# Optimization experiments

Measured on AMD Instinct MI355X. Metric: run time of the kernel, lower is better.

## Reference

```python
import jax, jax.numpy as jnp
import numpy as np

B, N, D, H, C = 32, 2048, 64, 4, 16  # batch, nodes, hidden, heads, per-head node-emb dim


def setup_inputs() -> dict:
    key = jax.random.key(0)
    ks = jax.random.split(key, 8)
    def w(k, shape):
        return jax.random.normal(k, shape, jnp.float32) * 0.05
    return {
        "hidden_state": jax.random.normal(ks[0], (B, N, D), jnp.float32),
        # predefined (row-normalized-ish) adjacencies; /N keeps 2-hop propagation magnitudes sane
        "A1": jax.random.uniform(ks[1], (N, N), jnp.float32) / N,
        "A2": jax.random.uniform(ks[2], (N, N), jnp.float32) / N,
        "E1": jax.random.normal(ks[3], (N, H, C), jnp.float32),
        "E2": jax.random.normal(ks[4], (N, H, C), jnp.float32),
        # GCNLayer mlp: Linear((gdep+1)*D, D) for z, r, c gates
        "Wz": w(ks[5], (3 * D, D)), "bz": jnp.zeros((D,), jnp.float32),
        "Wr": w(ks[6], (3 * D, D)), "br": jnp.zeros((D,), jnp.float32),
        "Wc": w(ks[7], (3 * D, D)), "bc": jnp.zeros((D,), jnp.float32),
        "w_pre": jnp.float32(0.5),
        "w_adp": jnp.float32(0.5),
    }


def _gcn2(A, x, W, b):
    h1 = jnp.einsum('wv,bvc->bwc', A, x)
    h2 = jnp.einsum('wv,bvc->bwc', A, h1)
    return jnp.concatenate([x, h1, h2], axis=-1) @ W + b


def _gcn3(A, x, W, b):
    # GCNLayer with per-head adjacency A:[H,N,N]; x broadcast to [B,H,N,D]
    h0 = jnp.broadcast_to(x[:, None], (x.shape[0], A.shape[0], x.shape[1], x.shape[2]))
    h1 = jnp.einsum('hwv,bhvc->bhwc', A, h0)
    h2 = jnp.einsum('hwv,bhvc->bhwc', A, h1)
    return jnp.concatenate([h0, h1, h2], axis=-1) @ W + b  # [B,H,N,D]


def reference(hidden_state, A1, A2, E1, E2, Wz, bz, Wr, br, Wc, bc, w_pre, w_adp):
    # adaptive attention-like adjacency: relu(E1 E2^T)/sqrt(c), softmax over v
    sqrt_c = jnp.sqrt(jnp.asarray(E1.shape[-1], jnp.float32))
    scores = jax.nn.relu(jnp.einsum('whc,vhc->hwv', E1, E2)) / sqrt_c  # [H,N,N]
    A_adp = jax.nn.softmax(scores, axis=-1)

    def gate(x, W, b):
        pre = _gcn2(A1, x, W, b) + _gcn2(A2, x, W, b)          # sum over predefined adjs
        adp = _gcn3(A_adp, x, W, b).mean(axis=1)               # mean over heads
        return w_pre * pre + w_adp * adp

    z = jax.nn.sigmoid(gate(hidden_state, Wz, bz))
    r = jax.nn.sigmoid(gate(hidden_state, Wr, br))
    c = jnp.tanh(gate(r * hidden_state, Wc, bc))
    return (1.0 - z) * hidden_state + z * c
```

## Files before the change

### kernel.cpp

```cpp
#include <hip/hip_runtime.h>

#define NNODE 2048
#define NBATCH 32

typedef __attribute__((ext_vector_type(4))) float f32x4;
typedef __attribute__((ext_vector_type(8))) __bf16 bf16x8;
typedef __attribute__((ext_vector_type(4))) __bf16 bf16x4;

__device__ __forceinline__ void gload16(const void* g, void* lds) {
  __builtin_amdgcn_global_load_lds(
      (const __attribute__((address_space(1))) unsigned int*)g,
      (__attribute__((address_space(3))) unsigned int*)lds, 16, 0, 0);
}

__global__ __launch_bounds__(256) void prep_ew(const float* __restrict__ E1,
                                               const float* __restrict__ E2,
                                               const float* __restrict__ Wz,
                                               const float* __restrict__ Wr,
                                               const float* __restrict__ Wc,
                                               const float* __restrict__ wpre,
                                               const float* __restrict__ wadp,
                                               __bf16* __restrict__ E1p,
                                               __bf16* __restrict__ E2p,
                                               __bf16* __restrict__ Wzrt,
                                               __bf16* __restrict__ Wct) {
  if (blockIdx.x < 128) {
    int idx = blockIdx.x * 256 + threadIdx.x;
    int cq = idx & 3;
    int n = (idx >> 2) & 2047;
    int h = idx >> 13;
    const float4 q1 = *(const float4*)(E1 + (size_t)(n * 4 + h) * 16 + cq * 4);
    const float4 q2 = *(const float4*)(E2 + (size_t)(n * 4 + h) * 16 + cq * 4);
    size_t o = ((size_t)h * NNODE + n) * 32 + cq * 4;
    E1p[o + 0] = (__bf16)q1.x; E1p[o + 1] = (__bf16)q1.y;
    E1p[o + 2] = (__bf16)q1.z; E1p[o + 3] = (__bf16)q1.w;
    E2p[o + 0] = (__bf16)q2.x; E2p[o + 1] = (__bf16)q2.y;
    E2p[o + 2] = (__bf16)q2.z; E2p[o + 3] = (__bf16)q2.w;
    size_t oz = o + 16;
    E1p[oz + 0] = (__bf16)0.f; E1p[oz + 1] = (__bf16)0.f;
    E1p[oz + 2] = (__bf16)0.f; E1p[oz + 3] = (__bf16)0.f;
    E2p[oz + 0] = (__bf16)0.f; E2p[oz + 1] = (__bf16)0.f;
    E2p[oz + 2] = (__bf16)0.f; E2p[oz + 3] = (__bf16)0.f;
  } else {
    int idx = (blockIdx.x - 128) * 256 + threadIdx.x;
    int rr = idx / 192, k = idx % 192;
    float s = 2.f * (*wpre) + (*wadp);
    float sc = (k < 64) ? s : 1.f;
    float vz = (rr < 64) ? Wz[(size_t)k * 64 + rr] : Wr[(size_t)k * 64 + rr - 64];
    Wzrt[idx] = (__bf16)(vz * sc);
    float vc = (rr < 64) ? Wc[(size_t)k * 64 + rr] * sc : 0.f;
    Wct[idx] = (__bf16)vc;
  }
}

__global__ __launch_bounds__(256) void score_gemm(const __bf16* __restrict__ E1p,
                                                  const __bf16* __restrict__ E2p,
                                                  __bf16* __restrict__ SC) {
  __shared__ __bf16 As[128 * 32];
  __shared__ __bf16 Bs[128 * 32];
  const int tid = threadIdx.x;
  const int wave = tid >> 6, lane = tid & 63;
  const int wr = wave >> 1, wc = wave & 1;
  const int h = blockIdx.z;
  const int m0 = blockIdx.x * 128, n0 = blockIdx.y * 128;
  const __bf16* A = E1p + (size_t)h * NNODE * 32;
  const __bf16* Bt = E2p + (size_t)h * NNODE * 32;
  const int rowA = tid >> 2;
  const int colb = (tid & 3) * 16;
  gload16((const char*)(A + (size_t)(m0 + rowA) * 32) + colb, (char*)As + wave * 1024);
  gload16((const char*)(A + (size_t)(m0 + rowA + 64) * 32) + colb, (char*)As + 4096 + wave * 1024);
  gload16((const char*)(Bt + (size_t)(n0 + rowA) * 32) + colb, (char*)Bs + wave * 1024);
  gload16((const char*)(Bt + (size_t)(n0 + rowA + 64) * 32) + colb, (char*)Bs + 4096 + wave * 1024);
  __syncthreads();

  f32x4 acc[4][4] = {};
  bf16x8 af[4], bfr[4];
#pragma unroll
  for (int mi = 0; mi < 4; ++mi)
    af[mi] = *(const bf16x8*)((const char*)As +
             ((wr * 64 + mi * 16 + (lane & 15)) * 64 + (lane >> 4) * 16));
#pragma unroll
  for (int ni = 0; ni < 4; ++ni)
    bfr[ni] = *(const bf16x8*)((const char*)Bs +
             ((wc * 64 + ni * 16 + (lane & 15)) * 64 + (lane >> 4) * 16));
#pragma unroll
  for (int mi = 0; mi < 4; ++mi)
#pragma unroll
    for (int ni = 0; ni < 4; ++ni)
      acc[mi][ni] = __builtin_amdgcn_mfma_f32_16x16x32_bf16(af[mi], bfr[ni],
                                                            acc[mi][ni], 0, 0, 0);

  const int crow = (lane >> 4) * 4;
  const int ccol = lane & 15;
#pragma unroll
  for (int mi = 0; mi < 4; ++mi)
#pragma unroll
    for (int ni = 0; ni < 4; ++ni) {
      int r0 = m0 + wr * 64 + mi * 16 + crow;
      int cc = n0 + wc * 64 + ni * 16 + ccol;
#pragma unroll
      for (int r = 0; r < 4; ++r) {
        float val = fmaxf(acc[mi][ni][r], 0.f) * 0.25f;
        SC[((size_t)h * NNODE + r0 + r) * NNODE + cc] = (__bf16)val;
      }
    }
}

__global__ __launch_bounds__(256) void soft_tx(const __bf16* __restrict__ SC,
                                               unsigned char* __restrict__ ADJ8,
                                               const float* __restrict__ x,
                                               unsigned char* __restrict__ XT8,
                                               __bf16* __restrict__ xbf) {
  const int tid = threadIdx.x;
  const size_t NN2 = (size_t)NNODE * NNODE;
  if (blockIdx.x < 2048) {
    const int wave = tid >> 6, lane = tid & 63;
    const size_t row = (size_t)blockIdx.x * 4 + wave;
    const __bf16* src = SC + row * NNODE;
    unsigned char* dst = ADJ8 + 2 * NN2 + row * NNODE;
    float v[32];
    float mx = 0.f;
#pragma unroll
    for (int j = 0; j < 4; ++j) {
      bf16x8 q = *(const bf16x8*)(src + j * 512 + lane * 8);
#pragma unroll
      for (int i = 0; i < 8; ++i) {
        float f = (float)q[i];
        v[j * 8 + i] = f;
        mx = fmaxf(mx, f);
      }
    }
#pragma unroll
    for (int o = 32; o > 0; o >>= 1) mx = fmaxf(mx, __shfl_xor(mx, o));
    float s = 0.f;
#pragma unroll
    for (int i = 0; i < 32; ++i) {
      v[i] = __expf(v[i] - mx);
      s += v[i];
    }
#pragma unroll
    for (int o = 32; o > 0; o >>= 1) s += __shfl_xor(s, o);
    float inv = 128.f / s;
#pragma unroll
    for (int j = 0; j < 4; ++j) {
      int w0 = __builtin_amdgcn_cvt_pk_fp8_f32(v[j * 8 + 0] * inv, v[j * 8 + 1] * inv, 0, false);
      w0 = __builtin_amdgcn_cvt_pk_fp8_f32(v[j * 8 + 2] * inv, v[j * 8 + 3] * inv, w0, true);
      int w1 = __builtin_amdgcn_cvt_pk_fp8_f32(v[j * 8 + 4] * inv, v[j * 8 + 5] * inv, 0, false);
      w1 = __builtin_amdgcn_cvt_pk_fp8_f32(v[j * 8 + 6] * inv, v[j * 8 + 7] * inv, w1, true);
      int2 pk; pk.x = w0; pk.y = w1;
      *(int2*)(dst + j * 512 + lane * 8) = pk;
    }
  } else {
    const int idx = blockIdx.x - 2048;
    const int b = idx >> 5, v0 = (idx & 31) * 64;
    __shared__ float t[64][65];
    const int vr = tid >> 2, c0 = (tid & 3) * 16;
    const float* src = x + ((size_t)b * NNODE + v0 + vr) * 64 + c0;
    __bf16* xb = xbf + ((size_t)b * NNODE + v0 + vr) * 64 + c0;
#pragma unroll
    for (int j = 0; j < 4; ++j) {
      float4 q = ((const float4*)src)[j];
      t[vr][c0 + j * 4 + 0] = q.x;
      t[vr][c0 + j * 4 + 1] = q.y;
      t[vr][c0 + j * 4 + 2] = q.z;
      t[vr][c0 + j * 4 + 3] = q.w;
      xb[j * 4 + 0] = (__bf16)q.x;
      xb[j * 4 + 1] = (__bf16)q.y;
      xb[j * 4 + 2] = (__bf16)q.z;
      xb[j * 4 + 3] = (__bf16)q.w;
    }
    __syncthreads();
    const float SX = 16.f;
#pragma unroll
    for (int jr = 0; jr < 4; ++jr) {
      int c = jr * 16 + (tid >> 4);
      int vq = (tid & 15) * 4;
      int w0 = __builtin_amdgcn_cvt_pk_fp8_f32(t[vq][c] * SX, t[vq + 1][c] * SX, 0, false);
      w0 = __builtin_amdgcn_cvt_pk_fp8_f32(t[vq + 2][c] * SX, t[vq + 3][c] * SX, w0, true);
      *(int*)(XT8 + ((size_t)(b * 64 + c)) * NNODE + v0 + vq) = w0;
    }
  }
}

__global__ __launch_bounds__(256) void prep_adj(const float* __restrict__ A1,
                                                const float* __restrict__ A2,
                                                unsigned char* __restrict__ ADJ8,
                                                unsigned char* __restrict__ ADJT8,
                                                unsigned char* __restrict__ M18,
                                                const float* __restrict__ wpre,
                                                const float* __restrict__ wadp) {
  const int r0 = blockIdx.x * 64, c0 = blockIdx.y * 64;
  const int tid = threadIdx.x;
  const size_t NN2 = (size_t)NNODE * NNODE;
  const float wp = *wpre, wa = *wadp * 0.25f;
  const float SA = 128.f;
  __shared__ float t[64][65];
  const int vr = tid >> 2, cg = (tid & 3) * 16;
  float m1acc[16] = {};

  for (int z = 0; z < 6; ++z) {
    const float wz = (z < 2) ? wp : wa;
    float vv[16];
    if (z < 2) {
      const float* src = (z == 0 ? A1 : A2) + (size_t)(r0 + vr) * NNODE + c0 + cg;
#pragma unroll
      for (int j = 0; j < 4; ++j) {
        float4 q = ((const float4*)src)[j];
        vv[j * 4 + 0] = q.x * SA; vv[j * 4 + 1] = q.y * SA;
        vv[j * 4 + 2] = q.z * SA; vv[j * 4 + 3] = q.w * SA;
      }
      int4 pk;
#pragma unroll
      for (int q = 0; q < 4; ++q) {
        int w0 = __builtin_amdgcn_cvt_pk_fp8_f32(vv[4 * q], vv[4 * q + 1], 0, false);
        w0 = __builtin_amdgcn_cvt_pk_fp8_f32(vv[4 * q + 2], vv[4 * q + 3], w0, true);
        (&pk.x)[q] = w0;
      }
      *(int4*)(ADJ8 + (size_t)z * NN2 + (size_t)(r0 + vr) * NNODE + c0 + cg) = pk;
    } else {
      int4 pk = *(const int4*)(ADJ8 + (size_t)z * NN2 + (size_t)(r0 + vr) * NNODE + c0 + cg);
#pragma unroll
      for (int q = 0; q < 4; ++q) {
        int w0 = (&pk.x)[q];
        vv[4 * q + 0] = __builtin_amdgcn_cvt_f32_fp8(w0, 0);
        vv[4 * q + 1] = __builtin_amdgcn_cvt_f32_fp8(w0, 1);
        vv[4 * q + 2] = __builtin_amdgcn_cvt_f32_fp8(w0, 2);
        vv[4 * q + 3] = __builtin_amdgcn_cvt_f32_fp8(w0, 3);
      }
    }
#pragma unroll
    for (int i = 0; i < 16; ++i) {
      m1acc[i] += wz * vv[i];
      t[vr][cg + i] = vv[i];
    }
    __syncthreads();
    {
#pragma unroll
      for (int jr = 0; jr < 4; ++jr) {
        int c = jr * 16 + (tid >> 4);
        int vq = (tid & 15) * 4;
        int w0 = __builtin_amdgcn_cvt_pk_fp8_f32(t[vq][c] * wz, t[vq + 1][c] * wz, 0, false);
        w0 = __builtin_amdgcn_cvt_pk_fp8_f32(t[vq + 2][c] * wz, t[vq + 3][c] * wz, w0, true);
        *(int*)(ADJT8 + (size_t)z * NN2 + (size_t)(c0 + c) * NNODE + r0 + vq) = w0;
      }
    }
    __syncthreads();
  }
  {
    int4 pk;
#pragma unroll
    for (int q = 0; q < 4; ++q) {
      int w0 = __builtin_amdgcn_cvt_pk_fp8_f32(m1acc[4 * q], m1acc[4 * q + 1], 0, false);
      w0 = __builtin_amdgcn_cvt_pk_fp8_f32(m1acc[4 * q + 2], m1acc[4 * q + 3], w0, true);
      (&pk.x)[q] = w0;
    }
    *(int4*)(M18 + (size_t)(r0 + vr) * NNODE + c0 + cg) = pk;
  }
}

#define VMCNT0() asm volatile("s_waitcnt vmcnt(0)" ::: "memory")
#define VMCNT4() asm volatile("s_waitcnt vmcnt(4)" ::: "memory")
#define LGKMCNT0() asm volatile("s_waitcnt lgkmcnt(0)" ::: "memory")
#define BARRIER() asm volatile("s_barrier" ::: "memory")

#define READFRAGS8(d, AF, BF)                                                 \
  do {                                                                        \
    _Pragma("unroll")                                                         \
    for (int mi = 0; mi < 4; ++mi) {                                          \
      AF[mi][0] = *(const long*)(AREG8(d) + aoff[mi][0]);                     \
      AF[mi][1] = *(const long*)(AREG8(d) + aoff[mi][1]);                     \
    }                                                                         \
    _Pragma("unroll")                                                         \
    for (int j = 0; j < 4; ++j) {                                             \
      BF[j][0] = *(const long*)(BREG8(d) + boff[j][0]);                       \
      BF[j][1] = *(const long*)(BREG8(d) + boff[j][1]);                       \
    }                                                                         \
  } while (0)

#define MFMA8(AF, BF)                                                         \
  do {                                                                        \
    __builtin_amdgcn_s_setprio(1);                                            \
    _Pragma("unroll")                                                         \
    for (int mi = 0; mi < 4; ++mi)                                            \
      _Pragma("unroll")                                                       \
      for (int j = 0; j < 4; ++j)                                             \
        _Pragma("unroll")                                                     \
        for (int ks = 0; ks < 2; ++ks)                                        \
          acc[mi][j] = __builtin_amdgcn_mfma_f32_16x16x32_fp8_fp8(            \
              AF[mi][ks], BF[j][ks], acc[mi][j], 0, 0, 0);                    \
    __builtin_amdgcn_s_setprio(0);                                            \
  } while (0)

#define FP8_GEOM()                                                            \
  int aoff[4][2], boff[4][2];                                                 \
  _Pragma("unroll")                                                           \
  for (int mi = 0; mi < 4; ++mi)                                              \
    _Pragma("unroll")                                                         \
    for (int ks = 0; ks < 2; ++ks) {                                          \
      int rh = mi * 32 + wr * 16 + (l & 15);                                  \
      int lo = rh * 64 + ks * 32 + ((l >> 4) * 8);                            \
      aoff[mi][ks] = lo ^ ((rh & 6) << 3);                                    \
    }                                                                         \
  _Pragma("unroll")                                                           \
  for (int j = 0; j < 4; ++j)                                                 \
    _Pragma("unroll")                                                         \
    for (int ks = 0; ks < 2; ++ks) {                                          \
      int rh = j * 32 + wc * 16 + (l & 15);                                   \
      int lo = rh * 64 + ks * 32 + ((l >> 4) * 8);                            \
      boff[j][ks] = lo ^ ((rh & 6) << 3);                                     \
    }                                                                         \
  const int sg_col = (((l & 3) ^ ((l >> 3) & 3)) << 4);                       \
  unsigned aLoff[2], bLoff[2];                                                \
  _Pragma("unroll")                                                           \
  for (int p = 0; p < 2; ++p) {                                               \
    int srow = p * 64 + w * 16 + (l >> 2);                                    \
    aLoff[p] = (unsigned)((m0 + srow) * 2048 + sg_col);                       \
    bLoff[p] = (unsigned)((n0 + srow) * 2048 + sg_col);                       \
  }

__global__ __launch_bounds__(256, 3) void gemm_sq(const unsigned char* __restrict__ ADJ8,
                                                  const unsigned char* __restrict__ ADJT8,
                                                  __bf16* __restrict__ M2part) {
  extern __shared__ char smem[];
  const int tid = threadIdx.x;
  const int w = tid >> 6, l = tid & 63;
  const int wr = w >> 1, wc = w & 1;
  const size_t NN2 = (size_t)NNODE * NNODE;
  int lin = blockIdx.x + 16 * blockIdx.y + 256 * blockIdx.z;
  int nlin = (lin & 7) * 96 + (lin >> 3);
  const int m0 = (nlin & 15) * 128, n0 = ((nlin >> 4) & 15) * 128;
  const int zh = nlin >> 8;
  const int zb = zh * 2;
  __bf16* Cp = M2part + (size_t)zh * NN2;
  const int NTT = 64;

#define AREG8(d) (smem + (d) * 8192)
#define BREG8(d) (smem + 16384 + (d) * 8192)

  FP8_GEOM();

#define STAGE8A(toff, region)                                                 \
  do {                                                                        \
    _Pragma("unroll")                                                         \
    for (int p = 0; p < 2; ++p)                                               \
      gload16((const char*)ADJ8 + (toff) + aLoff[p],                          \
              (region) + p * 4096 + w * 1024);                                \
  } while (0)
#define STAGE8B(toff, region)                                                 \
  do {                                                                        \
    _Pragma("unroll")                                                         \
    for (int p = 0; p < 2; ++p)                                               \
      gload16((const char*)ADJT8 + (toff) + bLoff[p],                         \
              (region) + p * 4096 + w * 1024);                                \
  } while (0)

  f32x4 acc[4][4] = {};
  long afA[4][2], bfA[4][2], afB[4][2], bfB[4][2];

  size_t tOff = (size_t)zb * NN2;
  STAGE8A(tOff, AREG8(0));
  STAGE8B(tOff, BREG8(0));
  STAGE8A(tOff + 64, AREG8(1));
  STAGE8B(tOff + 64, BREG8(1));
  tOff += 128;
  VMCNT4();
  BARRIER();
  READFRAGS8(0, afA, bfA);
  LGKMCNT0();
  BARRIER();

  for (int t = 0; t <= NTT - 4; t += 2) {
    STAGE8A(tOff, AREG8(0));
    STAGE8B(tOff, BREG8(0));
    tOff += (((t + 2) & 31) == 31) ? (NN2 - (size_t)31 * 64) : (size_t)64;
    VMCNT4();
    BARRIER();
    READFRAGS8(1, afB, bfB);
    MFMA8(afA, bfA);
    LGKMCNT0();
    BARRIER();
    STAGE8A(tOff, AREG8(1));
    STAGE8B(tOff, BREG8(1));
    tOff += (((t + 3) & 31) == 31) ? (NN2 - (size_t)31 * 64) : (size_t)64;
    VMCNT4();
    BARRIER();
    READFRAGS8(0, afA, bfA);
    MFMA8(afB, bfB);
    LGKMCNT0();
    BARRIER();
  }
  VMCNT0();
  BARRIER();
  READFRAGS8(1, afB, bfB);
  MFMA8(afA, bfA);
  LGKMCNT0();
  MFMA8(afB, bfB);

  const float DS = 1.f / 16384.f;
  const int crow = (l >> 4) * 4;
  const int ccol = l & 15;
#pragma unroll
  for (int mi = 0; mi < 4; ++mi)
#pragma unroll
    for (int j = 0; j < 4; ++j) {
      int r0 = m0 + mi * 32 + wr * 16 + crow;
      int cc = n0 + j * 32 + wc * 16 + ccol;
#pragma unroll
      for (int r = 0; r < 4; ++r)
        Cp[(size_t)(r0 + r) * NNODE + cc] = (__bf16)(acc[mi][j][r] * DS);
    }
#undef STAGE8A
#undef STAGE8B
#undef AREG8
#undef BREG8
}

__global__ __launch_bounds__(256, 3) void gemm_hop1s8(const unsigned char* __restrict__ XT8,
                                                      const unsigned char* __restrict__ M18,
                                                      const unsigned char* __restrict__ M28,
                                                      __bf16* __restrict__ S1,
                                                      __bf16* __restrict__ S2) {
  extern __shared__ char smem[];
  const int tid = threadIdx.x;
  const int w = tid >> 6, l = tid & 63;
  const int wr = w >> 1, wc = w & 1;
  int lin = blockIdx.x + 16 * blockIdx.y + 256 * blockIdx.z;
  int nlin = (lin & 7) * 64 + (lin >> 3);
  const int m0 = (nlin & 15) * 128, n0 = ((nlin >> 4) & 15) * 128;
  const int z = nlin >> 8;
  const unsigned char* Bbase = z ? M28 : M18;
  const int NT = NNODE / 64;

#define AREG8(d) (smem + (d) * 8192)
#define BREG8(d) (smem + 16384 + (d) * 8192)

  FP8_GEOM();

#define STAGE8A(koff, region)                                                 \
  do {                                                                        \
    _Pragma("unroll")                                                         \
    for (int p = 0; p < 2; ++p)                                               \
      gload16((const char*)XT8 + (koff) + aLoff[p],                           \
              (region) + p * 4096 + w * 1024);                                \
  } while (0)
#define STAGE8B(koff, region)                                                 \
  do {                                                                        \
    _Pragma("unroll")                                                         \
    for (int p = 0; p < 2; ++p)                                               \
      gload16((const char*)Bbase + (koff) + bLoff[p],                         \
              (region) + p * 4096 + w * 1024);                                \
  } while (0)

  f32x4 acc[4][4] = {};
  long afA[4][2], bfA[4][2], afB[4][2], bfB[4][2];

  size_t kOff = 0;
  STAGE8A(kOff, AREG8(0));
  STAGE8B(kOff, BREG8(0));
  STAGE8A(kOff + 64, AREG8(1));
  STAGE8B(kOff + 64, BREG8(1));
  kOff += 128;
  VMCNT4();
  BARRIER();
  READFRAGS8(0, afA, bfA);
  LGKMCNT0();
  BARRIER();

  for (int t = 0; t <= NT - 4; t += 2) {
    STAGE8A(kOff, AREG8(0));
    STAGE8B(kOff, BREG8(0));
    kOff += 64;
    VMCNT4();
    BARRIER();
    READFRAGS8(1, afB, bfB);
    MFMA8(afA, bfA);
    LGKMCNT0();
    BARRIER();
    STAGE8A(kOff, AREG8(1));
    STAGE8B(kOff, BREG8(1));
    kOff += 64;
    VMCNT4();
    BARRIER();
    READFRAGS8(0, afA, bfA);
    MFMA8(afB, bfB);
    LGKMCNT0();
    BARRIER();
  }
  VMCNT0();
  BARRIER();
  READFRAGS8(1, afB, bfB);
  MFMA8(afA, bfA);
  LGKMCNT0();
  MFMA8(afB, bfB);

  {
    __syncthreads();
    const float DS = 1.f / 2048.f;
    const int crow = (l >> 4) * 4;
    const int ccol = l & 15;
    char* T = smem;
#pragma unroll
    for (int mi = 0; mi < 4; ++mi)
#pragma unroll
      for (int j = 0; j < 4; ++j) {
        int ml = mi * 32 + wr * 16 + crow;
        int nl = j * 32 + wc * 16 + ccol;
        bf16x4 v;
#pragma unroll
        for (int r = 0; r < 4; ++r) v[r] = (__bf16)(acc[mi][j][r] * DS);
        *(bf16x4*)(T + nl * 256 + ((ml * 2) ^ ((nl & 7) << 4))) = v;
      }
    __syncthreads();
    __bf16* dst = z ? S2 : S1;
    const int bA = m0 >> 6;
#pragma unroll
    for (int it = 0; it < 4; ++it) {
      int nl = (tid >> 3) + it * 32;
      int seg = tid & 7;
      int xorv = (nl & 7) << 4;
      const char* src = T + nl * 256;
      bf16x8 v0 = *(const bf16x8*)(src + ((seg * 32) ^ xorv));
      bf16x8 v1 = *(const bf16x8*)(src + ((seg * 32 + 16) ^ xorv));
      int b = bA + (seg >> 2);
      size_t o = ((size_t)b * NNODE + n0 + nl) * 64 + (seg & 3) * 16;
      *(bf16x8*)(dst + o) = v0;
      *(bf16x8*)(dst + o + 8) = v1;
    }
  }
#undef STAGE8A
#undef STAGE8B
#undef AREG8
#undef BREG8
}

__global__ __launch_bounds__(256) void combine_m2(const __bf16* __restrict__ M2p,
                                                  unsigned char* __restrict__ M28) {
  const size_t NN2 = (size_t)NNODE * NNODE;
  size_t i = ((size_t)blockIdx.x * 256 + threadIdx.x) * 8;
  bf16x8 a = *(const bf16x8*)(M2p + i);
  bf16x8 b = *(const bf16x8*)(M2p + NN2 + i);
  bf16x8 c = *(const bf16x8*)(M2p + 2 * NN2 + i);
  const float SA = 128.f;
  float sv[8];
#pragma unroll
  for (int k = 0; k < 8; ++k)
    sv[k] = ((float)a[k] + (float)b[k] + (float)c[k]) * SA;
  int w0 = __builtin_amdgcn_cvt_pk_fp8_f32(sv[0], sv[1], 0, false);
  w0 = __builtin_amdgcn_cvt_pk_fp8_f32(sv[2], sv[3], w0, true);
  int w1 = __builtin_amdgcn_cvt_pk_fp8_f32(sv[4], sv[5], 0, false);
  w1 = __builtin_amdgcn_cvt_pk_fp8_f32(sv[6], sv[7], w1, true);
  int2 pk; pk.x = w0; pk.y = w1;
  *(int2*)(M28 + i) = pk;
}

template <int MODE>
__global__ __launch_bounds__(256) void gemm_lin(const __bf16* __restrict__ Xp,
                                                const __bf16* __restrict__ S1,
                                                const __bf16* __restrict__ S2,
                                                const __bf16* __restrict__ Wt,
                                                const float* __restrict__ b0,
                                                const float* __restrict__ b1,
                                                const float* __restrict__ wpre,
                                                const float* __restrict__ wadp,
                                                const float* __restrict__ hid,
                                                float* __restrict__ zbuf,
                                                __bf16* __restrict__ rxout,
                                                unsigned char* __restrict__ XT8out,
                                                float* __restrict__ outp) {
  __shared__ __bf16 As[128 * 32];
  __shared__ __bf16 Bs[128 * 32];
  __shared__ char T[64 * 256];
  const int tid = threadIdx.x;
  const int wave = tid >> 6, lane = tid & 63;
  const int wr = wave >> 1, wc = wave & 1;
  const int m0 = blockIdx.x * 128;
  const int rowA = tid >> 2;
  const int colb = (tid & 3) * 16;
  const __bf16* srcs[3] = {Xp, S1, S2};
  char* asD0 = (char*)As + wave * 1024;
  char* asD1 = (char*)As + 4096 + wave * 1024;
  char* bsD0 = (char*)Bs + wave * 1024;
  char* bsD1 = (char*)Bs + 4096 + wave * 1024;

  f32x4 acc[4][4] = {};

#pragma unroll
  for (int kt = 0; kt < 6; ++kt) {
    const __bf16* Ab = srcs[kt >> 1];
    const char* aS0 = (const char*)(Ab + (size_t)(m0 + rowA) * 64) + (kt & 1) * 64 + colb;
    const char* aS1 = (const char*)(Ab + (size_t)(m0 + rowA + 64) * 64) + (kt & 1) * 64 + colb;
    const char* bS0 = (const char*)(Wt + (size_t)rowA * 192) + kt * 64 + colb;
    const char* bS1 = (const char*)(Wt + (size_t)(rowA + 64) * 192) + kt * 64 + colb;
    gload16(aS0, asD0);
    gload16(aS1, asD1);
    gload16(bS0, bsD0);
    gload16(bS1, bsD1);
    __syncthreads();
    bf16x8 af[4], bfr[4];
#pragma unroll
    for (int mi = 0; mi < 4; ++mi)
      af[mi] = *(const bf16x8*)((const char*)As +
               ((wr * 64 + mi * 16 + (lane & 15)) * 64 + (lane >> 4) * 16));
#pragma unroll
    for (int ni = 0; ni < 4; ++ni)
      bfr[ni] = *(const bf16x8*)((const char*)Bs +
               ((wc * 64 + ni * 16 + (lane & 15)) * 64 + (lane >> 4) * 16));
#pragma unroll
    for (int mi = 0; mi < 4; ++mi)
#pragma unroll
      for (int ni = 0; ni < 4; ++ni)
        acc[mi][ni] = __builtin_amdgcn_mfma_f32_16x16x32_bf16(af[mi], bfr[ni],
                                                              acc[mi][ni], 0, 0, 0);
    __syncthreads();
  }

  const float wp = *wpre, wa = *wadp;
  const float s = 2.f * wp + wa;
  const int crow = (lane >> 4) * 4;
  const int ccol = lane & 15;
#pragma unroll
  for (int mi = 0; mi < 4; ++mi)
#pragma unroll
    for (int ni = 0; ni < 4; ++ni) {
      int r0 = m0 + wr * 64 + mi * 16 + crow;
      int col = wc * 64 + ni * 16 + ccol;
      int cf = col & 63;
      if (MODE == 0) {
        if (col < 64) {
#pragma unroll
          for (int r = 0; r < 4; ++r) {
            int row = r0 + r;
            float g = acc[mi][ni][r] + s * b0[cf];
            zbuf[(size_t)row * 64 + cf] = 1.f / (1.f + __expf(-g));
          }
        } else {
          bf16x4 tv;
#pragma unroll
          for (int r = 0; r < 4; ++r) {
            int row = r0 + r;
            float g = acc[mi][ni][r] + s * b1[cf];
            float rv = 1.f / (1.f + __expf(-g));
            __bf16 rxv = (__bf16)(rv * hid[(size_t)row * 64 + cf]);
            rxout[(size_t)row * 64 + cf] = rxv;
            tv[r] = rxv;
          }
          int vl0 = wr * 64 + mi * 16 + crow;
          *(bf16x4*)(T + cf * 256 + ((vl0 * 2) ^ ((cf & 7) << 4))) = tv;
        }
      } else {
        if (col < 64) {
#pragma unroll
          for (int r = 0; r < 4; ++r) {
            int row = r0 + r;
            float g = acc[mi][ni][r] + s * b0[cf];
            float cv = 1.f - 2.f / (1.f + __expf(2.f * g));
            float zv = zbuf[(size_t)row * 64 + cf];
            float hv = hid[(size_t)row * 64 + cf];
            outp[(size_t)row * 64 + cf] = (1.f - zv) * hv + zv * cv;
          }
        }
      }
    }

  if (MODE == 0) {
    __syncthreads();
    const int b = m0 >> 11;
    const int v0 = m0 & 2047;
    const float SX = 16.f;
#pragma unroll
    for (int it = 0; it < 4; ++it) {
      int rr = it * 16 + (tid >> 4);
      int seg = tid & 15;
      bf16x8 v = *(const bf16x8*)(T + rr * 256 + ((seg * 16) ^ ((rr & 7) << 4)));
      int w0 = __builtin_amdgcn_cvt_pk_fp8_f32((float)v[0] * SX, (float)v[1] * SX, 0, false);
      w0 = __builtin_amdgcn_cvt_pk_fp8_f32((float)v[2] * SX, (float)v[3] * SX, w0, true);
      int w1 = __builtin_amdgcn_cvt_pk_fp8_f32((float)v[4] * SX, (float)v[5] * SX, 0, false);
      w1 = __builtin_amdgcn_cvt_pk_fp8_f32((float)v[6] * SX, (float)v[7] * SX, w1, true);
      int2 pk; pk.x = w0; pk.y = w1;
      *(int2*)(XT8out + ((size_t)(b * 64 + rr)) * NNODE + v0 + seg * 8) = pk;
    }
  }
}

extern "C" void kernel_launch(void* const* d_in, const int* in_sizes, int n_in,
                              void* d_out, int out_size, void* d_ws, size_t ws_size,
                              hipStream_t stream) {
  (void)in_sizes; (void)n_in; (void)out_size;
  const float* x    = (const float*)d_in[0];
  const float* A1   = (const float*)d_in[1];
  const float* A2   = (const float*)d_in[2];
  const float* E1   = (const float*)d_in[3];
  const float* E2   = (const float*)d_in[4];
  const float* Wz   = (const float*)d_in[5];
  const float* bz   = (const float*)d_in[6];
  const float* Wr   = (const float*)d_in[7];
  const float* br   = (const float*)d_in[8];
  const float* Wc   = (const float*)d_in[9];
  const float* bc   = (const float*)d_in[10];
  const float* wpre = (const float*)d_in[11];
  const float* wadp = (const float*)d_in[12];
  float* out = (float*)d_out;

  char* ws = (char*)d_ws;
  const size_t NN2 = (size_t)NNODE * NNODE;
  const size_t NN2B = NN2 * 2;
  unsigned char* ADJ8  = (unsigned char*)(ws + 6 * NN2B);
  unsigned char* ADJT8 = (unsigned char*)(ws + 6 * NN2B + 6 * NN2);
  __bf16* SC   = (__bf16*)(ws + 12 * NN2B);
  __bf16* M2p  = (__bf16*)(ws + 12 * NN2B);
  unsigned char* M18 = (unsigned char*)(ws + 18 * NN2B);
  unsigned char* M28 = (unsigned char*)(ws + 18 * NN2B + NN2);
  unsigned char* XT8 = (unsigned char*)(ws + 20 * NN2B);
  __bf16* xbf  = (__bf16*)(ws + 21 * NN2B);
  __bf16* rx   = (__bf16*)(ws + 22 * NN2B);
  __bf16* S1   = (__bf16*)(ws + 2 * NN2B);
  __bf16* S2   = (__bf16*)(ws + 3 * NN2B);
  float*  zbuf = (float*)(ws + 4 * NN2B);
  __bf16* E1p  = (__bf16*)(ws + 23 * NN2B);
  __bf16* E2p  = E1p + 4 * NNODE * 32;
  __bf16* Wzrt = E2p + 4 * NNODE * 32;
  __bf16* Wct  = Wzrt + 128 * 192;
  if (ws_size < 23 * NN2B + 2 * 4 * NNODE * 32 * 2 + 2 * 128 * 192 * 2) return;

  prep_ew<<<224, 256, 0, stream>>>(E1, E2, Wz, Wr, Wc, wpre, wadp,
                                   E1p, E2p, Wzrt, Wct);
  score_gemm<<<dim3(16, 16, 4), 256, 0, stream>>>(E1p, E2p, SC);
  soft_tx<<<3072, 256, 0, stream>>>(SC, ADJ8, x, XT8, xbf);
  prep_adj<<<dim3(32, 32), 256, 0, stream>>>(A1, A2, ADJ8, ADJT8, M18,
                                             wpre, wadp);

  gemm_sq<<<dim3(16, 16, 3), 256, 32768, stream>>>(ADJ8, ADJT8, M2p);
  combine_m2<<<2048, 256, 0, stream>>>(M2p, M28);

  gemm_hop1s8<<<dim3(16, 16, 2), 256, 32768, stream>>>(XT8, M18, M28, S1, S2);
  gemm_lin<0><<<512, 256, 0, stream>>>(xbf, S1, S2, Wzrt, bz, br, wpre, wadp,
                                       x, zbuf, rx, XT8, nullptr);

  gemm_hop1s8<<<dim3(16, 16, 2), 256, 32768, stream>>>(XT8, M18, M28, S1, S2);
  gemm_lin<1><<<512, 256, 0, stream>>>(rx, S1, S2, Wct, bc, nullptr, wpre, wadp,
                                       x, zbuf, nullptr, nullptr, out);
}
```

Measured before the change: 199.9 us.

## Use scaled fp8 16x16x128 MFMA in gemm_sq with 128-wide K tiles and 2-way split-K

Switches the adjacency-squaring GEMM from the older fp8 MFMA path to the gfx950 scaled f8f6f4 16x16x128 MFMA with unit scales, doubling the K tile to 128 bytes and the LDS footprint to 64 KB with a new swizzle. Split-K drops from 3 partitions to 2, so each block does 48 K-steps and combine_m2 reads one fewer partial buffer. The goal is higher MFMA throughput and fewer k-iterations and barriers. In exchange occupancy falls from 3 to 2 blocks per CU and the grid launches fewer blocks.

Result: faster. 177.4 us (-11.3%).

```diff
diff --git a/kernel.cpp b/kernel.cpp
--- a/kernel.cpp
+++ b/kernel.cpp
@@ -6,6 +6,8 @@
 typedef __attribute__((ext_vector_type(4))) float f32x4;
 typedef __attribute__((ext_vector_type(8))) __bf16 bf16x8;
 typedef __attribute__((ext_vector_type(4))) __bf16 bf16x4;
+typedef __attribute__((ext_vector_type(4))) int i32x4;
+typedef __attribute__((ext_vector_type(8))) int i32x8;
 
 __device__ __forceinline__ void gload16(const void* g, void* lds) {
   __builtin_amdgcn_global_load_lds(
@@ -260,6 +262,7 @@
 
 #define VMCNT0() asm volatile("s_waitcnt vmcnt(0)" ::: "memory")
 #define VMCNT4() asm volatile("s_waitcnt vmcnt(4)" ::: "memory")
+#define VMCNT8() asm volatile("s_waitcnt vmcnt(8)" ::: "memory")
 #define LGKMCNT0() asm volatile("s_waitcnt lgkmcnt(0)" ::: "memory")
 #define BARRIER() asm volatile("s_barrier" ::: "memory")
 
@@ -318,7 +321,7 @@
     bLoff[p] = (unsigned)((n0 + srow) * 2048 + sg_col);                       \
   }
 
-__global__ __launch_bounds__(256, 3) void gemm_sq(const unsigned char* __restrict__ ADJ8,
+__global__ __launch_bounds__(256, 2) void gemm_sq(const unsigned char* __restrict__ ADJ8,
                                                   const unsigned char* __restrict__ ADJT8,
                                                   __bf16* __restrict__ M2part) {
   extern __shared__ char smem[];
@@ -327,74 +330,127 @@
   const int wr = w >> 1, wc = w & 1;
   const size_t NN2 = (size_t)NNODE * NNODE;
   int lin = blockIdx.x + 16 * blockIdx.y + 256 * blockIdx.z;
-  int nlin = (lin & 7) * 96 + (lin >> 3);
+  int nlin = (lin & 7) * 64 + (lin >> 3);
   const int m0 = (nlin & 15) * 128, n0 = ((nlin >> 4) & 15) * 128;
   const int zh = nlin >> 8;
-  const int zb = zh * 2;
+  const int zb = zh * 3;
   __bf16* Cp = M2part + (size_t)zh * NN2;
-  const int NTT = 64;
-
-#define AREG8(d) (smem + (d) * 8192)
-#define BREG8(d) (smem + 16384 + (d) * 8192)
-
-  FP8_GEOM();
-
-#define STAGE8A(toff, region)                                                 \
+  const int NTT = 48;
+
+#define AREG(d) (smem + (d) * 16384)
+#define BREG(d) (smem + 32768 + (d) * 16384)
+
+  int aoff[4][2], boff[4][2];
+#pragma unroll
+  for (int mi = 0; mi < 4; ++mi)
+#pragma unroll
+    for (int part = 0; part < 2; ++part) {
+      int rh = mi * 32 + wr * 16 + (l & 15);
+      int lo = rh * 128 + (l >> 4) * 32 + part * 16;
+      aoff[mi][part] = lo ^ ((rh & 7) << 4);
+    }
+#pragma unroll
+  for (int j = 0; j < 4; ++j)
+#pragma unroll
+    for (int part = 0; part < 2; ++part) {
+      int rh = j * 32 + wc * 16 + (l & 15);
+      int lo = rh * 128 + (l >> 4) * 32 + part * 16;
+      boff[j][part] = lo ^ ((rh & 7) << 4);
+    }
+
+  const int sg_row = w * 8 + (l >> 3);
+  const int sg_col = (((l & 7) ^ ((l >> 3) & 7)) << 4);
+  unsigned aLoff[4], bLoff[4];
+#pragma unroll
+  for (int p = 0; p < 4; ++p) {
+    aLoff[p] = (unsigned)((m0 + p * 32 + sg_row) * 2048 + sg_col);
+    bLoff[p] = (unsigned)((n0 + p * 32 + sg_row) * 2048 + sg_col);
+  }
+
+#define STAGEXA(toff, region)                                                 \
   do {                                                                        \
     _Pragma("unroll")                                                         \
-    for (int p = 0; p < 2; ++p)                                               \
+    for (int p = 0; p < 4; ++p)                                               \
       gload16((const char*)ADJ8 + (toff) + aLoff[p],                          \
               (region) + p * 4096 + w * 1024);                                \
   } while (0)
-#define STAGE8B(toff, region)                                                 \
+#define STAGEXB(toff, region)                                                 \
   do {                                                                        \
     _Pragma("unroll")                                                         \
-    for (int p = 0; p < 2; ++p)                                               \
+    for (int p = 0; p < 4; ++p)                                               \
       gload16((const char*)ADJT8 + (toff) + bLoff[p],                         \
               (region) + p * 4096 + w * 1024);                                \
   } while (0)
 
+#define RDFRAG(region, o0, o1)                                                \
+  __builtin_shufflevector(*(const i32x4*)((region) + (o0)),                   \
+                          *(const i32x4*)((region) + (o1)),                   \
+                          0, 1, 2, 3, 4, 5, 6, 7)
+
+#define READFRAGSX(d, AF, BF)                                                 \
+  do {                                                                        \
+    _Pragma("unroll")                                                         \
+    for (int mi = 0; mi < 4; ++mi)                                            \
+      AF[mi] = RDFRAG(AREG(d), aoff[mi][0], aoff[mi][1]);                     \
+    _Pragma("unroll")                                                         \
+    for (int j = 0; j < 4; ++j)                                               \
+      BF[j] = RDFRAG(BREG(d), boff[j][0], boff[j][1]);                        \
+  } while (0)
+
+  const int SC1 = 0x7F7F7F7F;
+#define MFMAX(AF, BF)                                                         \
+  do {                                                                        \
+    __builtin_amdgcn_s_setprio(1);                                            \
+    _Pragma("unroll")                                                         \
+    for (int mi = 0; mi < 4; ++mi)                                            \
+      _Pragma("unroll")                                                       \
+      for (int j = 0; j < 4; ++j)                                             \
+        acc[mi][j] = __builtin_amdgcn_mfma_scale_f32_16x16x128_f8f6f4(        \
+            AF[mi], BF[j], acc[mi][j], 0, 0, 0, SC1, 0, SC1);                 \
+    __builtin_amdgcn_s_setprio(0);                                            \
+  } while (0)
+
   f32x4 acc[4][4] = {};
-  long afA[4][2], bfA[4][2], afB[4][2], bfB[4][2];
+  i32x8 afA[4], bfA[4], afB[4], bfB[4];
 
   size_t tOff = (size_t)zb * NN2;
-  STAGE8A(tOff, AREG8(0));
-  STAGE8B(tOff, BREG8(0));
-  STAGE8A(tOff + 64, AREG8(1));
-  STAGE8B(tOff + 64, BREG8(1));
-  tOff += 128;
-  VMCNT4();
+  STAGEXA(tOff, AREG(0));
+  STAGEXB(tOff, BREG(0));
+  STAGEXA(tOff + 128, AREG(1));
+  STAGEXB(tOff + 128, BREG(1));
+  tOff += 256;
+  VMCNT8();
   BARRIER();
-  READFRAGS8(0, afA, bfA);
+  READFRAGSX(0, afA, bfA);
   LGKMCNT0();
   BARRIER();
 
   for (int t = 0; t <= NTT - 4; t += 2) {
-    STAGE8A(tOff, AREG8(0));
-    STAGE8B(tOff, BREG8(0));
-    tOff += (((t + 2) & 31) == 31) ? (NN2 - (size_t)31 * 64) : (size_t)64;
-    VMCNT4();
+    STAGEXA(tOff, AREG(0));
+    STAGEXB(tOff, BREG(0));
+    tOff += (((t + 2) & 15) == 15) ? (NN2 - (size_t)15 * 128) : (size_t)128;
+    VMCNT8();
     BARRIER();
-    READFRAGS8(1, afB, bfB);
-    MFMA8(afA, bfA);
+    READFRAGSX(1, afB, bfB);
+    MFMAX(afA, bfA);
     LGKMCNT0();
     BARRIER();
-    STAGE8A(tOff, AREG8(1));
-    STAGE8B(tOff, BREG8(1));
-    tOff += (((t + 3) & 31) == 31) ? (NN2 - (size_t)31 * 64) : (size_t)64;
-    VMCNT4();
+    STAGEXA(tOff, AREG(1));
+    STAGEXB(tOff, BREG(1));
+    tOff += (((t + 3) & 15) == 15) ? (NN2 - (size_t)15 * 128) : (size_t)128;
+    VMCNT8();
     BARRIER();
-    READFRAGS8(0, afA, bfA);
-    MFMA8(afB, bfB);
+    READFRAGSX(0, afA, bfA);
+    MFMAX(afB, bfB);
     LGKMCNT0();
     BARRIER();
   }
   VMCNT0();
   BARRIER();
-  READFRAGS8(1, afB, bfB);
-  MFMA8(afA, bfA);
+  READFRAGSX(1, afB, bfB);
+  MFMAX(afA, bfA);
   LGKMCNT0();
-  MFMA8(afB, bfB);
+  MFMAX(afB, bfB);
 
   const float DS = 1.f / 16384.f;
   const int crow = (l >> 4) * 4;
@@ -409,10 +465,13 @@
       for (int r = 0; r < 4; ++r)
         Cp[(size_t)(r0 + r) * NNODE + cc] = (__bf16)(acc[mi][j][r] * DS);
     }
-#undef STAGE8A
-#undef STAGE8B
-#undef AREG8
-#undef BREG8
+#undef STAGEXA
+#undef STAGEXB
+#undef RDFRAG
+#undef READFRAGSX
+#undef MFMAX
+#undef AREG
+#undef BREG
 }
 
 __global__ __launch_bounds__(256, 3) void gemm_hop1s8(const unsigned char* __restrict__ XT8,
@@ -539,12 +598,11 @@
   size_t i = ((size_t)blockIdx.x * 256 + threadIdx.x) * 8;
   bf16x8 a = *(const bf16x8*)(M2p + i);
   bf16x8 b = *(const bf16x8*)(M2p + NN2 + i);
-  bf16x8 c = *(const bf16x8*)(M2p + 2 * NN2 + i);
   const float SA = 128.f;
   float sv[8];
 #pragma unroll
   for (int k = 0; k < 8; ++k)
-    sv[k] = ((float)a[k] + (float)b[k] + (float)c[k]) * SA;
+    sv[k] = ((float)a[k] + (float)b[k]) * SA;
   int w0 = __builtin_amdgcn_cvt_pk_fp8_f32(sv[0], sv[1], 0, false);
   w0 = __builtin_amdgcn_cvt_pk_fp8_f32(sv[2], sv[3], w0, true);
   int w1 = __builtin_amdgcn_cvt_pk_fp8_f32(sv[4], sv[5], 0, false);
@@ -729,7 +787,7 @@
   prep_adj<<<dim3(32, 32), 256, 0, stream>>>(A1, A2, ADJ8, ADJT8, M18,
                                              wpre, wadp);
 
-  gemm_sq<<<dim3(16, 16, 3), 256, 32768, stream>>>(ADJ8, ADJT8, M2p);
+  gemm_sq<<<dim3(16, 16, 2), 256, 65536, stream>>>(ADJ8, ADJT8, M2p);
   combine_m2<<<2048, 256, 0, stream>>>(M2p, M28);
 
   gemm_hop1s8<<<dim3(16, 16, 2), 256, 32768, stream>>>(XT8, M18, M28, S1, S2);
```
